# Performance work log

Measured on AMD Instinct MI355X. Metric: run time of the kernel, lower is better.

Reference implementation:

```python
import jax, jax.numpy as jnp
import numpy as np
from functools import partial

U, I, D, E = 8192, 8192, 128, 524288
N = U + I


def setup_inputs() -> dict:
    key = jax.random.key(0)
    ks = jax.random.split(key, 12)
    s = 1.0 / np.sqrt(D)
    return {
        "user_emb": jax.random.normal(ks[0], (U, D), jnp.float32) * 0.1,
        "item_emb": jax.random.normal(ks[1], (I, D), jnp.float32) * 0.1,
        "adj_rows": jax.random.randint(ks[2], (E,), 0, N, jnp.int32),
        "adj_cols": jax.random.randint(ks[3], (E,), 0, N, jnp.int32),
        "adj_vals": jax.random.uniform(ks[4], (E,), jnp.float32) * (1.0 / 32.0),
        "wq": jax.random.normal(ks[5], (D, D), jnp.float32) * s,
        "bq": jnp.zeros((D,), jnp.float32),
        "wk": jax.random.normal(ks[6], (D, D), jnp.float32) * s,
        "bk": jnp.zeros((D,), jnp.float32),
        "wv": jax.random.normal(ks[7], (D, D), jnp.float32) * s,
        "bv": jnp.zeros((D,), jnp.float32),
        "fw": jax.random.normal(ks[8], (D, D), jnp.float32) * s,
        "fb": jnp.zeros((D,), jnp.float32),
        "n_layers": 3,
        "topk": 32,
    }


def _spmm(vals, rows, cols, x):
    # sparse [N,N] @ dense [N,D] via gather + segment_sum
    return jax.ops.segment_sum(vals[:, None] * x[cols], rows, num_segments=N)


def reference(user_emb, item_emb, adj_rows, adj_cols, adj_vals,
              wq, bq, wk, bk, wv, bv, fw, fb, n_layers, topk):
    ego = jnp.concatenate([user_emb, item_emb], axis=0)  # [N, D]
    layers = []
    for _ in range(n_layers):
        ego = _spmm(adj_vals, adj_rows, adj_cols, ego)
        layers.append(ego)
    all_emb = jnp.mean(jnp.stack(layers, axis=1), axis=1)  # [N, D]

    # full similarity + topk + gather
    sim = ego @ ego.T                                # [N, N]
    idx = jax.lax.top_k(sim, topk)[1]                # [N, K]
    samples = jnp.take(ego, idx, axis=0)             # [N, K, D]

    # per-node small attention over the K samples (dropout = eval identity)
    q = ego @ wq.T + bq                              # [N, D]
    k_ = samples @ wk.T + bk                         # [N, K, D]
    v = samples @ wv.T + bv                          # [N, K, D]
    scores = jnp.einsum('nd,nkd->nk', q, k_) / jnp.sqrt(jnp.float32(D))
    attn = jax.nn.softmax(scores, axis=-1)
    atten_embed = jnp.einsum('nk,nkd->nd', attn, v) + 0.1 * ego

    # fusion gating (softmax over dim=1, i.e. the node axis, as in source)
    a1 = jnp.tanh(all_emb @ fw.T + fb)
    a2 = jnp.tanh(atten_embed @ fw.T + fb)
    a = jax.nn.softmax(jnp.stack([a1, a2], axis=0), axis=1)  # [2, N, D]
    fusion = a[0] * all_emb + a[1] * atten_embed

    return (all_emb[:U], all_emb[U:],
            atten_embed[:U], atten_embed[U:],
            fusion[:U], fusion[U:])
```

## Files before the change

### kernel.cpp

```cpp
#include <hip/hip_runtime.h>
#include <math.h>

#define U_ 8192
#define I_ 8192
#define D_ 128
#define E_ 524288
#define N_ 16384
#define K_ 32
#define CAP_ 512

typedef unsigned short u16;
typedef unsigned int u32;
typedef unsigned long long u64;
typedef __attribute__((ext_vector_type(8))) short bf16x8;
typedef __attribute__((ext_vector_type(4))) float f32x4;

__global__ void k_init(const float* __restrict__ wq, const float* __restrict__ wk,
                       const float* __restrict__ bq, const float* __restrict__ wv,
                       const float* __restrict__ fw,
                       float* __restrict__ M, float* __restrict__ bqk,
                       float* __restrict__ wvT, float* __restrict__ fwdT,
                       int* __restrict__ cnt, float* __restrict__ cs1,
                       float* __restrict__ cs2,
                       float* __restrict__ svec, int* __restrict__ gcount,
                       int* __restrict__ failn) {
  const int tid = blockIdx.x * 256 + threadIdx.x;
  cnt[tid] = 0;
  gcount[tid] = 0;
  if (tid < 2048) { cs1[tid] = 0.f; cs2[tid] = 0.f; }
  if (tid < 128) svec[tid] = 0.f;
  if (tid == 0) *failn = 0;
  const int i = tid >> 7, j = tid & 127;
  float s = 0.f;
  for (int l = 0; l < 128; ++l) s += wq[l * 128 + i] * wk[l * 128 + j];
  M[tid] = s;
  wvT[i * 128 + j] = wv[j * 128 + i];
  fwdT[i * 128 + j] = fw[j * 128 + i];
  if (tid < 128) {
    float s2 = 0.f;
    for (int l = 0; l < 128; ++l) s2 += bq[l] * wk[l * 128 + tid];
    bqk[tid] = s2;
  }
}

__global__ void k_concat(const float* __restrict__ user, const float* __restrict__ item,
                         float* __restrict__ ego) {
  const int i = blockIdx.x * 256 + threadIdx.x;
  ego[i] = (i < U_ * D_) ? user[i] : item[i - U_ * D_];
}

__global__ void k_hist(const int* __restrict__ rows, int* __restrict__ cnt) {
  const int e = blockIdx.x * 256 + threadIdx.x;
  atomicAdd(&cnt[rows[e]], 1);
}

__global__ void k_scan(const int* __restrict__ cnt, int* __restrict__ row_ptr,
                       int* __restrict__ cursor) {
  __shared__ int wsum[16];
  __shared__ int carry_s;
  const int t = threadIdx.x;
  const int lane = t & 63, wid = t >> 6;
  if (t == 0) carry_s = 0;
  __syncthreads();
  for (int c = 0; c < N_ / 1024; ++c) {
    const int x = cnt[c * 1024 + t];
    int incl = x;
#pragma unroll
    for (int off = 1; off < 64; off <<= 1) {
      const int v = __shfl_up(incl, off, 64);
      if (lane >= off) incl += v;
    }
    if (lane == 63) wsum[wid] = incl;
    __syncthreads();
    if (wid == 0) {
      int s = (lane < 16) ? wsum[lane] : 0;
#pragma unroll
      for (int off = 1; off < 16; off <<= 1) {
        const int v = __shfl_up(s, off, 64);
        if (lane >= off) s += v;
      }
      if (lane < 16) wsum[lane] = s;
    }
    __syncthreads();
    const int carry = carry_s;
    const int wbase = wid ? wsum[wid - 1] : 0;
    const int excl = carry + wbase + incl - x;
    row_ptr[c * 1024 + t] = excl;
    cursor[c * 1024 + t] = excl;
    __syncthreads();
    if (t == 1023) carry_s += wsum[15];
    __syncthreads();
  }
  if (t == 0) row_ptr[N_] = carry_s;
}

__global__ void k_scatter(const int* __restrict__ rows, const int* __restrict__ cols,
                          const float* __restrict__ vals, int* __restrict__ cursor,
                          int* __restrict__ ccol, float* __restrict__ cval) {
  const int e = blockIdx.x * 256 + threadIdx.x;
  const int r = rows[e];
  const int p = atomicAdd(&cursor[r], 1);
  ccol[p] = cols[e];
  cval[p] = vals[e];
}

__global__ __launch_bounds__(128) void k_spmm(const float* __restrict__ x,
                                              float* __restrict__ y,
                                              float* __restrict__ sum,
                                              const int* __restrict__ row_ptr,
                                              const int* __restrict__ ccol,
                                              const float* __restrict__ cval,
                                              const int first, const int last) {
  const int r = blockIdx.x, d = threadIdx.x;
  const int b = row_ptr[r], e = row_ptr[r + 1];
  double a0 = 0.0, a1 = 0.0, a2 = 0.0, a3 = 0.0;
  int i = b;
  for (; i + 3 < e; i += 4) {
    a0 += (double)cval[i + 0] * (double)x[ccol[i + 0] * 128 + d];
    a1 += (double)cval[i + 1] * (double)x[ccol[i + 1] * 128 + d];
    a2 += (double)cval[i + 2] * (double)x[ccol[i + 2] * 128 + d];
    a3 += (double)cval[i + 3] * (double)x[ccol[i + 3] * 128 + d];
  }
  for (; i < e; ++i)
    a0 += (double)cval[i] * (double)x[ccol[i] * 128 + d];
  const float f = (float)((a0 + a1) + (a2 + a3));
  y[r * 128 + d] = f;
  float s = first ? f : sum[r * 128 + d] + f;
  if (last) s = s / 3.0f;
  sum[r * 128 + d] = s;
}

__global__ __launch_bounds__(256) void k_split_t(const float* __restrict__ x,
                                                 u16* __restrict__ Gh, u16* __restrict__ Gl,
                                                 u16* __restrict__ XTh, u16* __restrict__ XTl,
                                                 float* __restrict__ svec) {
  __shared__ u16 lh[128 * 66];
  __shared__ u16 ll[128 * 66];
  const int tid = threadIdx.x;
  const int r0 = blockIdx.x * 64;
  float colsum = 0.f;
  for (int s = 0; s < 32; ++s) {
    const int idx = tid + s * 256;
    const int r = idx >> 7, d = idx & 127;
    const float v = x[(r0 + r) * 128 + d];
    colsum += v;
    unsigned int u = __float_as_uint(v);
    u += 0x7fffu + ((u >> 16) & 1u);
    const u16 h = (u16)(u >> 16);
    const float hf = __uint_as_float(((unsigned int)h) << 16);
    const float l = v - hf;
    unsigned int u2 = __float_as_uint(l);
    u2 += 0x7fffu + ((u2 >> 16) & 1u);
    const u16 lo = (u16)(u2 >> 16);
    Gh[(r0 + r) * 128 + d] = h;
    Gl[(r0 + r) * 128 + d] = lo;
    lh[d * 66 + r] = h;
    ll[d * 66 + r] = lo;
  }
  atomicAdd(&svec[tid & 127], colsum);
  __syncthreads();
  for (int s = 0; s < 32; ++s) {
    const int idx = tid + s * 256;
    const int d = idx >> 6, rr = idx & 63;
    XTh[d * 16384 + r0 + rr] = lh[d * 66 + rr];
    XTl[d * 16384 + r0 + rr] = ll[d * 66 + rr];
  }
}

__global__ __launch_bounds__(256) void k_c2mfma(const u16* __restrict__ XTh,
                                                const u16* __restrict__ XTl,
                                                float* __restrict__ C2part) {
  const int tid = threadIdx.x, w = tid >> 6, lane = tid & 63;
  const int n16 = lane & 15, kq = lane >> 4;
  const int c0 = blockIdx.x * 64;
  f32x4 acc[2][8];
#pragma unroll
  for (int a = 0; a < 2; ++a)
#pragma unroll
    for (int b = 0; b < 8; ++b) acc[a][b] = (f32x4){0.f, 0.f, 0.f, 0.f};
  for (int ks = 0; ks < 2; ++ks) {
    const int c = c0 + ks * 32 + kq * 8;
    bf16x8 Fh[8], Fl[8];
#pragma unroll
    for (int g = 0; g < 8; ++g) {
      const int base = (g * 16 + n16) * 16384 + c;
      Fh[g] = *(const bf16x8*)&XTh[base];
      Fl[g] = *(const bf16x8*)&XTl[base];
    }
#pragma unroll
    for (int a = 0; a < 2; ++a) {
      const int tr = w * 2 + a;
#pragma unroll
      for (int b = 0; b < 8; ++b) {
        acc[a][b] = __builtin_amdgcn_mfma_f32_16x16x32_bf16(Fl[tr], Fh[b], acc[a][b], 0, 0, 0);
        acc[a][b] = __builtin_amdgcn_mfma_f32_16x16x32_bf16(Fh[tr], Fl[b], acc[a][b], 0, 0, 0);
        acc[a][b] = __builtin_amdgcn_mfma_f32_16x16x32_bf16(Fh[tr], Fh[b], acc[a][b], 0, 0, 0);
      }
    }
  }
  float* dst = C2part + (size_t)blockIdx.x * 16384;
#pragma unroll
  for (int a = 0; a < 2; ++a) {
    const int tr = w * 2 + a;
#pragma unroll
    for (int b = 0; b < 8; ++b)
#pragma unroll
      for (int i = 0; i < 4; ++i)
        dst[(tr * 16 + kq * 4 + i) * 128 + b * 16 + n16] = acc[a][b][i];
  }
}

__global__ void k_c2red(const float* __restrict__ C2part, float* __restrict__ C2) {
  const int e = blockIdx.x * 256 + threadIdx.x;
  float s = 0.f;
  for (int b = 0; b < 256; ++b) s += C2part[(size_t)b * 16384 + e];
  C2[e] = s;
}

__global__ __launch_bounds__(128) void k_tau(const float* __restrict__ x,
                                             const float* __restrict__ C2,
                                             const float* __restrict__ svec,
                                             float* __restrict__ tau) {
  __shared__ float xs[8][128];
  __shared__ double red[128];
  const int tid = threadIdx.x;
  const int n0 = blockIdx.x * 8;
#pragma unroll
  for (int rr = 0; rr < 8; ++rr) xs[rr][tid] = x[(n0 + rr) * 128 + tid];
  __syncthreads();
  double y[8];
#pragma unroll
  for (int rr = 0; rr < 8; ++rr) y[rr] = 0.0;
  for (int k2 = 0; k2 < 128; ++k2) {
    const double c = (double)C2[k2 * 128 + tid];
#pragma unroll
    for (int rr = 0; rr < 8; ++rr) y[rr] += (double)xs[rr][k2] * c;
  }
  const double sv = (double)svec[tid];
  for (int rr = 0; rr < 8; ++rr) {
    red[tid] = (double)xs[rr][tid] * y[rr];
    __syncthreads();
    for (int s = 64; s; s >>= 1) { if (tid < s) red[tid] += red[tid + s]; __syncthreads(); }
    const double exy = red[0] / 16384.0;
    __syncthreads();
    red[tid] = (double)xs[rr][tid] * sv;
    __syncthreads();
    for (int s = 64; s; s >>= 1) { if (tid < s) red[tid] += red[tid + s]; __syncthreads(); }
    if (tid == 0) {
      const double m = red[0] / 16384.0;
      double var = exy - m * m;
      if (var < 0.0) var = 0.0;
      tau[n0 + rr] = (float)(m + 2.55 * sqrt(var));
    }
    __syncthreads();
  }
}

__global__ __launch_bounds__(256) void k_qk(const float* __restrict__ ego,
                                            const float* __restrict__ M,
                                            const float* __restrict__ bqk,
                                            float* __restrict__ qkout) {
  __shared__ float xs[8][128];
  const int tid = threadIdx.x;
  const int r0 = blockIdx.x * 8;
#pragma unroll
  for (int s = 0; s < 4; ++s) {
    const int idx = tid + s * 256;
    xs[idx >> 7][idx & 127] = ego[r0 * 128 + idx];
  }
  __syncthreads();
  const int j = tid & 127, h = tid >> 7;
  const float bj = bqk[j];
  float acc[4];
#pragma unroll
  for (int r = 0; r < 4; ++r) acc[r] = bj;
  for (int d = 0; d < 128; d += 4) {
    const float w0 = M[(d + 0) * 128 + j];
    const float w1 = M[(d + 1) * 128 + j];
    const float w2 = M[(d + 2) * 128 + j];
    const float w3 = M[(d + 3) * 128 + j];
#pragma unroll
    for (int r = 0; r < 4; ++r) {
      const float4 xv = *(const float4*)&xs[h * 4 + r][d];
      acc[r] += xv.x * w0 + xv.y * w1 + xv.z * w2 + xv.w * w3;
    }
  }
#pragma unroll
  for (int r = 0; r < 4; ++r)
    qkout[(r0 + h * 4 + r) * 128 + j] = acc[r];
}

__device__ __forceinline__ void gload_lds16(const u16* g, u16* l) {
  __builtin_amdgcn_global_load_lds(
      (const __attribute__((address_space(1))) void*)g,
      (__attribute__((address_space(3))) void*)l, 16, 0, 0);
}

__global__ __launch_bounds__(256) void k_simmfma(const u16* __restrict__ Gh,
                                                 const u16* __restrict__ Gl,
                                                 const float* __restrict__ tau,
                                                 int* __restrict__ gstripcnt,
                                                 int2* __restrict__ gbuf) {
  __shared__ __align__(16) u16 lh[64 * 128];
  __shared__ int cnt128[128];
  const int tid = threadIdx.x;
  const int w = tid >> 6, lane = tid & 63;
  const int strip = blockIdx.x & 15, rgrp = blockIdx.x >> 4;
  const int n16 = lane & 15, kq = lane >> 4;

  if (tid < 128) cnt128[tid] = 0;

  const int rowbase = rgrp * 128 + w * 32;
  bf16x8 Bh[2][4], Bl[2][4];
#pragma unroll
  for (int rg = 0; rg < 2; ++rg) {
    const int row = rowbase + rg * 16 + n16;
#pragma unroll
    for (int q = 0; q < 4; ++q) {
      Bh[rg][q] = *(const bf16x8*)&Gh[row * 128 + q * 32 + kq * 8];
      Bl[rg][q] = *(const bf16x8*)&Gl[row * 128 + q * 32 + kq * 8];
    }
  }
  const float tau0 = tau[rowbase + n16];
  const float tau1 = tau[rowbase + 16 + n16];
  const int col0 = strip * 1024;

  for (int st = 0; st < 16; ++st) {
    const int cb = col0 + st * 64;
    __syncthreads();
#pragma unroll
    for (int ii = 0; ii < 4; ++ii) {
      const int srow = w * 16 + ii * 4 + kq;
      const int chunk = n16 ^ (srow & 7);
      gload_lds16(Gh + (((size_t)(cb + srow)) << 7) + chunk * 8,
                  lh + ((w * 16 + ii * 4) << 7));
    }
    __syncthreads();
#pragma unroll
    for (int ct = 0; ct < 4; ++ct) {
      const int ar = ct * 16 + n16;
      const char* lbase = (const char*)lh + ar * 256;
      bf16x8 Ah[4];
#pragma unroll
      for (int q = 0; q < 4; ++q)
        Ah[q] = *(const bf16x8*)(lbase + ((q * 64 + kq * 16) ^ ((ar & 7) << 4)));
#pragma unroll
      for (int rg = 0; rg < 2; ++rg) {
        f32x4 p = {0.f, 0.f, 0.f, 0.f};
        f32x4 r = {0.f, 0.f, 0.f, 0.f};
#pragma unroll
        for (int q = 0; q < 4; ++q) {
          p = __builtin_amdgcn_mfma_f32_16x16x32_bf16(Ah[q], Bh[rg][q], p, 0, 0, 0);
          r = __builtin_amdgcn_mfma_f32_16x16x32_bf16(Ah[q], Bl[rg][q], r, 0, 0, 0);
        }
        const float tv = rg ? tau1 : tau0;
        const int lrow = w * 32 + rg * 16 + n16;
        const int row = rgrp * 128 + lrow;
#pragma unroll
        for (int i = 0; i < 4; ++i) {
          const float v = p[i] + r[i];
          if (v > tv) {
            const int c = cb + ct * 16 + kq * 4 + i;
            const int pos = atomicAdd(&cnt128[lrow], 1);
            if (pos < 32)
              gbuf[row * CAP_ + strip * 32 + pos] = make_int2(c, __float_as_int(v));
          }
        }
      }
    }
  }
  __syncthreads();
  if (tid < 128) gstripcnt[(rgrp * 128 + tid) * 16 + strip] = cnt128[tid];
}

__global__ void k_check(const int* __restrict__ gstripcnt, int* __restrict__ failq,
                        int* __restrict__ failn) {
  const int n = blockIdx.x * 256 + threadIdx.x;
  int total = 0; int over = 0;
#pragma unroll
  for (int s = 0; s < 16; ++s) {
    const int c = gstripcnt[n * 16 + s];
    total += c;
    over |= (c > 32);
  }
  if (total < 36 || total > CAP_ || over) {
    const int s = atomicAdd(failn, 1);
    if (s < 64) failq[s] = n;
  }
}

__global__ __launch_bounds__(256) void k_refine(const int* __restrict__ gstripcnt,
                                                const int2* __restrict__ gbuf,
                                                int* __restrict__ topk_idx) {
  __shared__ u64 lk[4][CAP_];
  const int tid = threadIdx.x, w = tid >> 6, lane = tid & 63;
  const int n = blockIdx.x * 4 + w;

  const int scn = (lane < 16) ? gstripcnt[n * 16 + lane] : 0;
  int total = 0, over = 0;
#pragma unroll
  for (int s = 0; s < 16; ++s) {
    const int c = __shfl(scn, s, 64);
    total += c;
    over |= (c > 32);
  }
  const int bad = (total < 36 || total > CAP_ || over);
  const int cnt = bad ? 0 : total;

  int base = 0;
#pragma unroll
  for (int s = 0; s < 16; ++s) {
    const int c = __shfl(scn, s, 64);
    if (!bad && lane < c) {
      const int2 p = gbuf[n * CAP_ + s * 32 + lane];
      u32 uv = (u32)p.y;
      uv = (uv >> 31) ? ~uv : (uv | 0x80000000u);
      lk[w][base + lane] = ((u64)uv << 32) | (u64)(16383 - p.x);
    }
    base += bad ? 0 : c;
  }
  __syncthreads();

  for (int ci = lane; ci < cnt; ci += 64) {
    const u64 kk = lk[w][ci];
    int r = 0;
#pragma unroll 4
    for (int j = 0; j < cnt; ++j)
      r += (lk[w][j] > kk) ? 1 : 0;
    if (r < 32) topk_idx[n * 32 + r] = 16383 - (int)(u32)(kk & 0xffffffffu);
  }
  if (bad && lane < 32) topk_idx[n * 32 + lane] = 0;
}

__global__ __launch_bounds__(256) void k_fallback(const float* __restrict__ x,
                                                  const int* __restrict__ failq,
                                                  const int* __restrict__ failn,
                                                  double* __restrict__ fsim,
                                                  int* __restrict__ topk_idx) {
  const int nf = *failn;
  const int which = blockIdx.x;
  if (which >= nf || which >= 64) return;
  const int row = failq[which];
  __shared__ float xs[128];
  __shared__ double bm[256];
  __shared__ int bc[256];
  const int tid = threadIdx.x;
  if (tid < 128) xs[tid] = x[row * 128 + tid];
  __syncthreads();
  double* fs = fsim + (size_t)which * 16384;
  for (int c = tid; c < 16384; c += 256) {
    const float4* xp = (const float4*)&x[c * 128];
    double a = 0.0;
    for (int d = 0; d < 32; ++d) {
      const float4 v = xp[d];
      a += (double)xs[d * 4 + 0] * (double)v.x + (double)xs[d * 4 + 1] * (double)v.y +
           (double)xs[d * 4 + 2] * (double)v.z + (double)xs[d * 4 + 3] * (double)v.w;
    }
    fs[c] = a;
  }
  __syncthreads();
  for (int r = 0; r < 32; ++r) {
    double m = -1.0e300; int mc = 0;
    for (int c = tid; c < 16384; c += 256) {
      const double v = fs[c];
      if (v > m || (v == m && c < mc)) { m = v; mc = c; }
    }
    bm[tid] = m; bc[tid] = mc;
    __syncthreads();
    for (int s = 128; s; s >>= 1) {
      if (tid < s) {
        if (bm[tid + s] > bm[tid] || (bm[tid + s] == bm[tid] && bc[tid + s] < bc[tid])) {
          bm[tid] = bm[tid + s]; bc[tid] = bc[tid + s];
        }
      }
      __syncthreads();
    }
    if (tid == 0) { topk_idx[row * 32 + r] = bc[0]; fs[bc[0]] = -1.0e300; }
    __syncthreads();
  }
}

__global__ __launch_bounds__(128) void k_attn(const float* __restrict__ ego,
                                              float* __restrict__ qk,
                                              const int* __restrict__ topk_idx) {
  __shared__ float qv[128];
  __shared__ float sm[32 * 129];
  __shared__ int tki[32];
  __shared__ float sc[32];
  __shared__ float psum[128];
  const int n = blockIdx.x, tid = threadIdx.x;
  qv[tid] = qk[n * 128 + tid];
  if (tid < 32) tki[tid] = topk_idx[n * 32 + tid] & 16383;
  __syncthreads();
  for (int e = tid; e < 32 * 128; e += 128) {
    const int k2 = e >> 7, d = e & 127;
    sm[k2 * 129 + d] = ego[tki[k2] * 128 + d];
  }
  __syncthreads();
  {
    const int kk = tid & 31, part = tid >> 5;
    float s = 0.f;
    const int d0 = part * 32;
    for (int d = d0; d < d0 + 32; ++d) s += qv[d] * sm[kk * 129 + d];
    psum[tid] = s;
  }
  __syncthreads();
  if (tid < 32) {
    float v = psum[tid] + psum[tid + 32] + psum[tid + 64] + psum[tid + 96];
    v *= (1.0f / 11.313708498984760f);
    float m = v;
#pragma unroll
    for (int off = 16; off; off >>= 1) m = fmaxf(m, __shfl_xor(m, off, 32));
    const float e = expf(v - m);
    float ssum = e;
#pragma unroll
    for (int off = 16; off; off >>= 1) ssum += __shfl_xor(ssum, off, 32);
    sc[tid] = e / ssum;
  }
  __syncthreads();
  float sad = 0.f;
  for (int k2 = 0; k2 < 32; ++k2) sad += sc[k2] * sm[k2 * 129 + tid];
  qk[n * 128 + tid] = sad;
}

__global__ __launch_bounds__(256) void k_attnmm(const float* __restrict__ sa,
                                                const float* __restrict__ ego,
                                                const float* __restrict__ wvT,
                                                const float* __restrict__ bv,
                                                float* __restrict__ atten) {
  __shared__ float xs[8][128];
  const int tid = threadIdx.x;
  const int r0 = blockIdx.x * 8;
#pragma unroll
  for (int s = 0; s < 4; ++s) {
    const int idx = tid + s * 256;
    xs[idx >> 7][idx & 127] = sa[r0 * 128 + idx];
  }
  __syncthreads();
  const int j = tid & 127, h = tid >> 7;
  const float bj = bv[j];
  float acc[4];
#pragma unroll
  for (int r = 0; r < 4; ++r) acc[r] = bj;
  for (int d = 0; d < 128; d += 4) {
    const float w0 = wvT[(d + 0) * 128 + j];
    const float w1 = wvT[(d + 1) * 128 + j];
    const float w2 = wvT[(d + 2) * 128 + j];
    const float w3 = wvT[(d + 3) * 128 + j];
#pragma unroll
    for (int r = 0; r < 4; ++r) {
      const float4 xv = *(const float4*)&xs[h * 4 + r][d];
      acc[r] += xv.x * w0 + xv.y * w1 + xv.z * w2 + xv.w * w3;
    }
  }
#pragma unroll
  for (int r = 0; r < 4; ++r) {
    const int n = r0 + h * 4 + r;
    atten[n * 128 + j] = acc[r] + 0.1f * ego[n * 128 + j];
  }
}

__global__ __launch_bounds__(256) void k_fuse1(const float* __restrict__ allemb,
                                               const float* __restrict__ atten,
                                               const float* __restrict__ fwdT,
                                               const float* __restrict__ fb,
                                               float* __restrict__ z1,
                                               float* __restrict__ z2,
                                               float* __restrict__ cs1,
                                               float* __restrict__ cs2) {
  __shared__ float xs[8][128];
  __shared__ float as[8][128];
  __shared__ float red1[2][128];
  __shared__ float red2[2][128];
  const int tid = threadIdx.x;
  const int r0 = blockIdx.x * 8;
#pragma unroll
  for (int s = 0; s < 4; ++s) {
    const int idx = tid + s * 256;
    const int rr = idx >> 7, d = idx & 127;
    xs[rr][d] = allemb[(r0 + rr) * 128 + d];
    as[rr][d] = atten[(r0 + rr) * 128 + d];
  }
  __syncthreads();
  const int j = tid & 127, h = tid >> 7;
  const float fbj = fb[j];
  float acc1[4], acc2[4];
#pragma unroll
  for (int r = 0; r < 4; ++r) { acc1[r] = fbj; acc2[r] = fbj; }
  for (int d = 0; d < 128; d += 4) {
    const float w0 = fwdT[(d + 0) * 128 + j];
    const float w1 = fwdT[(d + 1) * 128 + j];
    const float w2 = fwdT[(d + 2) * 128 + j];
    const float w3 = fwdT[(d + 3) * 128 + j];
#pragma unroll
    for (int r = 0; r < 4; ++r) {
      const int rr = h * 4 + r;
      const float4 xv = *(const float4*)&xs[rr][d];
      const float4 av = *(const float4*)&as[rr][d];
      acc1[r] += xv.x * w0 + xv.y * w1 + xv.z * w2 + xv.w * w3;
      acc2[r] += av.x * w0 + av.y * w1 + av.z * w2 + av.w * w3;
    }
  }
  float ls1 = 0.f, ls2 = 0.f;
#pragma unroll
  for (int r = 0; r < 4; ++r) {
    const int rr = h * 4 + r;
    const float t1 = tanhf(acc1[r]);
    const float t2 = tanhf(acc2[r]);
    z1[(r0 + rr) * 128 + j] = t1;
    z2[(r0 + rr) * 128 + j] = t2;
    ls1 += expf(t1 - 1.0f);
    ls2 += expf(t2 - 1.0f);
  }
  red1[h][j] = ls1;
  red2[h][j] = ls2;
  __syncthreads();
  if (h == 0) {
    const int rep = blockIdx.x & 15;
    atomicAdd(&cs1[rep * 128 + j], red1[0][j] + red1[1][j]);
    atomicAdd(&cs2[rep * 128 + j], red2[0][j] + red2[1][j]);
  }
}

__global__ void k_fuse2(const float* __restrict__ allemb, const float* __restrict__ atten,
                        const float* __restrict__ z1, const float* __restrict__ z2,
                        const float* __restrict__ cs1, const float* __restrict__ cs2,
                        float* __restrict__ fusion) {
  __shared__ float s1[128], s2[128];
  const int tid = threadIdx.x;
  if (tid < 128) {
    float a = 0.f, b = 0.f;
#pragma unroll
    for (int rep = 0; rep < 16; ++rep) {
      a += cs1[rep * 128 + tid];
      b += cs2[rep * 128 + tid];
    }
    s1[tid] = a; s2[tid] = b;
  }
  __syncthreads();
  const int i = blockIdx.x * 256 + tid;
  const int j = i & 127;
  const float a1 = expf(z1[i] - 1.0f) / s1[j];
  const float a2 = expf(z2[i] - 1.0f) / s2[j];
  fusion[i] = a1 * allemb[i] + a2 * atten[i];
}

extern "C" void kernel_launch(void* const* d_in, const int* in_sizes, int n_in,
                              void* d_out, int out_size, void* d_ws, size_t ws_size,
                              hipStream_t stream) {
  (void)in_sizes; (void)n_in; (void)out_size; (void)ws_size;
  const float* user = (const float*)d_in[0];
  const float* item = (const float*)d_in[1];
  const int* adj_rows = (const int*)d_in[2];
  const int* adj_cols = (const int*)d_in[3];
  const float* adj_vals = (const float*)d_in[4];
  const float* wq = (const float*)d_in[5];
  const float* bq = (const float*)d_in[6];
  const float* wk = (const float*)d_in[7];
  const float* wv = (const float*)d_in[9];
  const float* bv = (const float*)d_in[10];
  const float* fw = (const float*)d_in[11];
  const float* fb = (const float*)d_in[12];

  float* out = (float*)d_out;
  float* allemb = out;
  float* atten = out + (size_t)N_ * D_;
  float* fusion = out + (size_t)2 * N_ * D_;

  char* ws = (char*)d_ws;
  size_t off = 0;
  auto alloc = [&](size_t bytes) { char* p = ws + off; off += (bytes + 255) & ~(size_t)255; return p; };
  float* ego_a = (float*)alloc((size_t)N_ * D_ * 4);
  float* ego_b = (float*)alloc((size_t)N_ * D_ * 4);
  float* qkbuf = (float*)alloc((size_t)N_ * D_ * 4);
  u16* Gh = (u16*)alloc((size_t)N_ * D_ * 2);
  u16* Gl = (u16*)alloc((size_t)N_ * D_ * 2);
  u16* XTh = (u16*)alloc((size_t)N_ * D_ * 2);
  u16* XTl = (u16*)alloc((size_t)N_ * D_ * 2);
  int2* gbuf = (int2*)alloc((size_t)N_ * CAP_ * 8);
  float* z1 = (float*)gbuf;
  float* z2 = (float*)alloc((size_t)N_ * D_ * 4);
  int* topk_idx = (int*)alloc((size_t)N_ * 32 * 4);
  int* ccol = (int*)alloc((size_t)E_ * 4);
  float* cval = (float*)alloc((size_t)E_ * 4);
  int* cnt = (int*)alloc((size_t)N_ * 4);
  int* row_ptr = (int*)alloc((size_t)(N_ + 1) * 4);
  int* cursor = (int*)alloc((size_t)N_ * 4);
  float* M = (float*)alloc(128 * 128 * 4);
  float* bqk = (float*)alloc(128 * 4);
  float* wvT = (float*)alloc(128 * 128 * 4);
  float* fwdT = (float*)alloc(128 * 128 * 4);
  float* cs1 = (float*)alloc(16 * 128 * 4);
  float* cs2 = (float*)alloc(16 * 128 * 4);
  float* C2 = (float*)alloc(128 * 128 * 4);
  float* C2part = (float*)alloc((size_t)256 * 16384 * 4);
  float* svec = (float*)alloc(128 * 4);
  float* tau = (float*)alloc((size_t)N_ * 4);
  int* gcount = (int*)alloc((size_t)N_ * 4);
  int* gstripcnt = (int*)alloc((size_t)N_ * 16 * 4);
  int* failq = (int*)alloc(64 * 4);
  int* failn = (int*)alloc(4);
  double* fsim = (double*)alloc((size_t)64 * N_ * 8);

  k_init<<<64, 256, 0, stream>>>(wq, wk, bq, wv, fw, M, bqk, wvT, fwdT, cnt, cs1, cs2, svec, gcount, failn);
  k_concat<<<8192, 256, 0, stream>>>(user, item, ego_a);
  k_hist<<<2048, 256, 0, stream>>>(adj_rows, cnt);
  k_scan<<<1, 1024, 0, stream>>>(cnt, row_ptr, cursor);
  k_scatter<<<2048, 256, 0, stream>>>(adj_rows, adj_cols, adj_vals, cursor, ccol, cval);

  k_spmm<<<N_, 128, 0, stream>>>(ego_a, ego_b, allemb, row_ptr, ccol, cval, 1, 0);
  k_spmm<<<N_, 128, 0, stream>>>(ego_b, ego_a, allemb, row_ptr, ccol, cval, 0, 0);
  k_spmm<<<N_, 128, 0, stream>>>(ego_a, ego_b, allemb, row_ptr, ccol, cval, 0, 1);

  k_split_t<<<256, 256, 0, stream>>>(ego_b, Gh, Gl, XTh, XTl, svec);
  k_c2mfma<<<256, 256, 0, stream>>>(XTh, XTl, C2part);
  k_c2red<<<64, 256, 0, stream>>>(C2part, C2);
  k_tau<<<2048, 128, 0, stream>>>(ego_b, C2, svec, tau);

  k_qk<<<2048, 256, 0, stream>>>(ego_b, M, bqk, qkbuf);
  k_simmfma<<<2048, 256, 0, stream>>>(Gh, Gl, tau, gstripcnt, gbuf);
  k_check<<<64, 256, 0, stream>>>(gstripcnt, failq, failn);
  k_refine<<<4096, 256, 0, stream>>>(gstripcnt, gbuf, topk_idx);
  k_fallback<<<64, 256, 0, stream>>>(ego_b, failq, failn, fsim, topk_idx);
  k_attn<<<N_, 128, 0, stream>>>(ego_b, qkbuf, topk_idx);
  k_attnmm<<<2048, 256, 0, stream>>>(qkbuf, ego_b, wvT, bv, atten);

  k_fuse1<<<2048, 256, 0, stream>>>(allemb, atten, fwdT, fb, z1, z2, cs1, cs2);
  k_fuse2<<<8192, 256, 0, stream>>>(allemb, atten, z1, z2, cs1, cs2, fusion);
}
```

Baseline: 687.1 us.

## Fuse small kernels, unroll SpMM by 8, and use shuffle reductions in tau

Several changes land together. The edge histogram moves into the concat kernel, the fail check moves into refine, and the attention V-projection is fused with the first fusion-gating kernel so atten is reused from LDS instead of being reloaded. The SpMM inner loop goes from 4 to 8 independent double accumulators to allow more gathers in flight. The tau kernel replaces per-row LDS tree reductions with wavefront shuffle reductions and a single barrier. The aim is to cut launch count, memory round-trips and barriers, at the cost of more registers in SpMM and a different floating-point summation order.

Measured after the change: 664.8 us. 1.03x faster.

```diff
diff --git a/kernel.cpp b/kernel.cpp
--- a/kernel.cpp
+++ b/kernel.cpp
@@ -44,14 +44,11 @@
 }
 
 __global__ void k_concat(const float* __restrict__ user, const float* __restrict__ item,
-                         float* __restrict__ ego) {
+                         float* __restrict__ ego,
+                         const int* __restrict__ rows, int* __restrict__ cnt) {
   const int i = blockIdx.x * 256 + threadIdx.x;
   ego[i] = (i < U_ * D_) ? user[i] : item[i - U_ * D_];
-}
-
-__global__ void k_hist(const int* __restrict__ rows, int* __restrict__ cnt) {
-  const int e = blockIdx.x * 256 + threadIdx.x;
-  atomicAdd(&cnt[rows[e]], 1);
+  if (i < E_) atomicAdd(&cnt[rows[i]], 1);
 }
 
 __global__ void k_scan(const int* __restrict__ cnt, int* __restrict__ row_ptr,
@@ -113,17 +110,18 @@
                                               const int first, const int last) {
   const int r = blockIdx.x, d = threadIdx.x;
   const int b = row_ptr[r], e = row_ptr[r + 1];
-  double a0 = 0.0, a1 = 0.0, a2 = 0.0, a3 = 0.0;
+  double a[8];
+#pragma unroll
+  for (int u = 0; u < 8; ++u) a[u] = 0.0;
   int i = b;
-  for (; i + 3 < e; i += 4) {
-    a0 += (double)cval[i + 0] * (double)x[ccol[i + 0] * 128 + d];
-    a1 += (double)cval[i + 1] * (double)x[ccol[i + 1] * 128 + d];
-    a2 += (double)cval[i + 2] * (double)x[ccol[i + 2] * 128 + d];
-    a3 += (double)cval[i + 3] * (double)x[ccol[i + 3] * 128 + d];
+  for (; i + 7 < e; i += 8) {
+#pragma unroll
+    for (int u = 0; u < 8; ++u)
+      a[u] += (double)cval[i + u] * (double)x[ccol[i + u] * 128 + d];
   }
   for (; i < e; ++i)
-    a0 += (double)cval[i] * (double)x[ccol[i] * 128 + d];
-  const float f = (float)((a0 + a1) + (a2 + a3));
+    a[0] += (double)cval[i] * (double)x[ccol[i] * 128 + d];
+  const float f = (float)((((a[0] + a[1]) + (a[2] + a[3])) + ((a[4] + a[5]) + (a[6] + a[7]))));
   y[r * 128 + d] = f;
   float s = first ? f : sum[r * 128 + d] + f;
   if (last) s = s / 3.0f;
@@ -222,8 +220,9 @@
                                              const float* __restrict__ svec,
                                              float* __restrict__ tau) {
   __shared__ float xs[8][128];
-  __shared__ double red[128];
+  __shared__ double r1[8][2], r2[8][2];
   const int tid = threadIdx.x;
+  const int lane = tid & 63, wid = tid >> 6;
   const int n0 = blockIdx.x * 8;
 #pragma unroll
   for (int rr = 0; rr < 8; ++rr) xs[rr][tid] = x[(n0 + rr) * 128 + tid];
@@ -237,22 +236,24 @@
     for (int rr = 0; rr < 8; ++rr) y[rr] += (double)xs[rr][k2] * c;
   }
   const double sv = (double)svec[tid];
+#pragma unroll
   for (int rr = 0; rr < 8; ++rr) {
-    red[tid] = (double)xs[rr][tid] * y[rr];
-    __syncthreads();
-    for (int s = 64; s; s >>= 1) { if (tid < s) red[tid] += red[tid + s]; __syncthreads(); }
-    const double exy = red[0] / 16384.0;
-    __syncthreads();
-    red[tid] = (double)xs[rr][tid] * sv;
-    __syncthreads();
-    for (int s = 64; s; s >>= 1) { if (tid < s) red[tid] += red[tid + s]; __syncthreads(); }
-    if (tid == 0) {
-      const double m = red[0] / 16384.0;
-      double var = exy - m * m;
-      if (var < 0.0) var = 0.0;
-      tau[n0 + rr] = (float)(m + 2.55 * sqrt(var));
-    }
-    __syncthreads();
+    double v1 = (double)xs[rr][tid] * y[rr];
+    double v2 = (double)xs[rr][tid] * sv;
+#pragma unroll
+    for (int off = 32; off; off >>= 1) {
+      v1 += __shfl_xor(v1, off, 64);
+      v2 += __shfl_xor(v2, off, 64);
+    }
+    if (lane == 0) { r1[rr][wid] = v1; r2[rr][wid] = v2; }
+  }
+  __syncthreads();
+  if (tid < 8) {
+    const double exy = (r1[tid][0] + r1[tid][1]) / 16384.0;
+    const double m = (r2[tid][0] + r2[tid][1]) / 16384.0;
+    double var = exy - m * m;
+    if (var < 0.0) var = 0.0;
+    tau[n0 + tid] = (float)(m + 2.55 * sqrt(var));
   }
 }
 
@@ -373,25 +374,11 @@
   if (tid < 128) gstripcnt[(rgrp * 128 + tid) * 16 + strip] = cnt128[tid];
 }
 
-__global__ void k_check(const int* __restrict__ gstripcnt, int* __restrict__ failq,
-                        int* __restrict__ failn) {
-  const int n = blockIdx.x * 256 + threadIdx.x;
-  int total = 0; int over = 0;
-#pragma unroll
-  for (int s = 0; s < 16; ++s) {
-    const int c = gstripcnt[n * 16 + s];
-    total += c;
-    over |= (c > 32);
-  }
-  if (total < 36 || total > CAP_ || over) {
-    const int s = atomicAdd(failn, 1);
-    if (s < 64) failq[s] = n;
-  }
-}
-
 __global__ __launch_bounds__(256) void k_refine(const int* __restrict__ gstripcnt,
                                                 const int2* __restrict__ gbuf,
-                                                int* __restrict__ topk_idx) {
+                                                int* __restrict__ topk_idx,
+                                                int* __restrict__ failq,
+                                                int* __restrict__ failn) {
   __shared__ u64 lk[4][CAP_];
   const int tid = threadIdx.x, w = tid >> 6, lane = tid & 63;
   const int n = blockIdx.x * 4 + w;
@@ -429,7 +416,13 @@
       r += (lk[w][j] > kk) ? 1 : 0;
     if (r < 32) topk_idx[n * 32 + r] = 16383 - (int)(u32)(kk & 0xffffffffu);
   }
-  if (bad && lane < 32) topk_idx[n * 32 + lane] = 0;
+  if (bad) {
+    if (lane == 0) {
+      const int s = atomicAdd(failn, 1);
+      if (s < 64) failq[s] = n;
+    }
+    if (lane < 32) topk_idx[n * 32 + lane] = 0;
+  }
 }
 
 __global__ __launch_bounds__(256) void k_fallback(const float* __restrict__ x,
@@ -523,53 +516,21 @@
   qk[n * 128 + tid] = sad;
 }
 
-__global__ __launch_bounds__(256) void k_attnmm(const float* __restrict__ sa,
-                                                const float* __restrict__ ego,
-                                                const float* __restrict__ wvT,
-                                                const float* __restrict__ bv,
-                                                float* __restrict__ atten) {
+__global__ __launch_bounds__(256) void k_attnfuse(const float* __restrict__ sa,
+                                                  const float* __restrict__ ego,
+                                                  const float* __restrict__ allemb,
+                                                  const float* __restrict__ wvT,
+                                                  const float* __restrict__ bv,
+                                                  const float* __restrict__ fwdT,
+                                                  const float* __restrict__ fb,
+                                                  float* __restrict__ atten,
+                                                  float* __restrict__ z1,
+                                                  float* __restrict__ z2,
+                                                  float* __restrict__ cs1,
+                                                  float* __restrict__ cs2) {
   __shared__ float xs[8][128];
-  const int tid = threadIdx.x;
-  const int r0 = blockIdx.x * 8;
-#pragma unroll
-  for (int s = 0; s < 4; ++s) {
-    const int idx = tid + s * 256;
-    xs[idx >> 7][idx & 127] = sa[r0 * 128 + idx];
-  }
-  __syncthreads();
-  const int j = tid & 127, h = tid >> 7;
-  const float bj = bv[j];
-  float acc[4];
-#pragma unroll
-  for (int r = 0; r < 4; ++r) acc[r] = bj;
-  for (int d = 0; d < 128; d += 4) {
-    const float w0 = wvT[(d + 0) * 128 + j];
-    const float w1 = wvT[(d + 1) * 128 + j];
-    const float w2 = wvT[(d + 2) * 128 + j];
-    const float w3 = wvT[(d + 3) * 128 + j];
-#pragma unroll
-    for (int r = 0; r < 4; ++r) {
-      const float4 xv = *(const float4*)&xs[h * 4 + r][d];
-      acc[r] += xv.x * w0 + xv.y * w1 + xv.z * w2 + xv.w * w3;
-    }
-  }
-#pragma unroll
-  for (int r = 0; r < 4; ++r) {
-    const int n = r0 + h * 4 + r;
-    atten[n * 128 + j] = acc[r] + 0.1f * ego[n * 128 + j];
-  }
-}
-
-__global__ __launch_bounds__(256) void k_fuse1(const float* __restrict__ allemb,
-                                               const float* __restrict__ atten,
-                                               const float* __restrict__ fwdT,
-                                               const float* __restrict__ fb,
-                                               float* __restrict__ z1,
-                                               float* __restrict__ z2,
-                                               float* __restrict__ cs1,
-                                               float* __restrict__ cs2) {
-  __shared__ float xs[8][128];
-  __shared__ float as[8][128];
+  __shared__ float xa[8][128];
+  __shared__ float as_[8][128];
   __shared__ float red1[2][128];
   __shared__ float red2[2][128];
   const int tid = threadIdx.x;
@@ -578,11 +539,36 @@
   for (int s = 0; s < 4; ++s) {
     const int idx = tid + s * 256;
     const int rr = idx >> 7, d = idx & 127;
-    xs[rr][d] = allemb[(r0 + rr) * 128 + d];
-    as[rr][d] = atten[(r0 + rr) * 128 + d];
+    xs[rr][d] = sa[(r0 + rr) * 128 + d];
+    xa[rr][d] = allemb[(r0 + rr) * 128 + d];
   }
   __syncthreads();
   const int j = tid & 127, h = tid >> 7;
+  {
+    const float bj = bv[j];
+    float acc[4];
+#pragma unroll
+    for (int r = 0; r < 4; ++r) acc[r] = bj;
+    for (int d = 0; d < 128; d += 4) {
+      const float w0 = wvT[(d + 0) * 128 + j];
+      const float w1 = wvT[(d + 1) * 128 + j];
+      const float w2 = wvT[(d + 2) * 128 + j];
+      const float w3 = wvT[(d + 3) * 128 + j];
+#pragma unroll
+      for (int r = 0; r < 4; ++r) {
+        const float4 xv = *(const float4*)&xs[h * 4 + r][d];
+        acc[r] += xv.x * w0 + xv.y * w1 + xv.z * w2 + xv.w * w3;
+      }
+    }
+#pragma unroll
+    for (int r = 0; r < 4; ++r) {
+      const int n = r0 + h * 4 + r;
+      const float av = acc[r] + 0.1f * ego[n * 128 + j];
+      atten[n * 128 + j] = av;
+      as_[h * 4 + r][j] = av;
+    }
+  }
+  __syncthreads();
   const float fbj = fb[j];
   float acc1[4], acc2[4];
 #pragma unroll
@@ -595,8 +581,8 @@
 #pragma unroll
     for (int r = 0; r < 4; ++r) {
       const int rr = h * 4 + r;
-      const float4 xv = *(const float4*)&xs[rr][d];
-      const float4 av = *(const float4*)&as[rr][d];
+      const float4 xv = *(const float4*)&xa[rr][d];
+      const float4 av = *(const float4*)&as_[rr][d];
       acc1[r] += xv.x * w0 + xv.y * w1 + xv.z * w2 + xv.w * w3;
       acc2[r] += av.x * w0 + av.y * w1 + av.z * w2 + av.w * w3;
     }
@@ -703,8 +689,7 @@
   double* fsim = (double*)alloc((size_t)64 * N_ * 8);
 
   k_init<<<64, 256, 0, stream>>>(wq, wk, bq, wv, fw, M, bqk, wvT, fwdT, cnt, cs1, cs2, svec, gcount, failn);
-  k_concat<<<8192, 256, 0, stream>>>(user, item, ego_a);
-  k_hist<<<2048, 256, 0, stream>>>(adj_rows, cnt);
+  k_concat<<<8192, 256, 0, stream>>>(user, item, ego_a, adj_rows, cnt);
   k_scan<<<1, 1024, 0, stream>>>(cnt, row_ptr, cursor);
   k_scatter<<<2048, 256, 0, stream>>>(adj_rows, adj_cols, adj_vals, cursor, ccol, cval);
 
@@ -719,12 +704,10 @@
 
   k_qk<<<2048, 256, 0, stream>>>(ego_b, M, bqk, qkbuf);
   k_simmfma<<<2048, 256, 0, stream>>>(Gh, Gl, tau, gstripcnt, gbuf);
-  k_check<<<64, 256, 0, stream>>>(gstripcnt, failq, failn);
-  k_refine<<<4096, 256, 0, stream>>>(gstripcnt, gbuf, topk_idx);
+  k_refine<<<4096, 256, 0, stream>>>(gstripcnt, gbuf, topk_idx, failq, failn);
   k_fallback<<<64, 256, 0, stream>>>(ego_b, failq, failn, fsim, topk_idx);
   k_attn<<<N_, 128, 0, stream>>>(ego_b, qkbuf, topk_idx);
-  k_attnmm<<<2048, 256, 0, stream>>>(qkbuf, ego_b, wvT, bv, atten);
-
-  k_fuse1<<<2048, 256, 0, stream>>>(allemb, atten, fwdT, fb, z1, z2, cs1, cs2);
+  k_attnfuse<<<2048, 256, 0, stream>>>(qkbuf, ego_b, allemb, wvT, bv, fwdT, fb,
+                                       atten, z1, z2, cs1, cs2);
   k_fuse2<<<8192, 256, 0, stream>>>(allemb, atten, z1, z2, cs1, cs2, fusion);
 }
```
